# Performance work log

Hardware: AMD Instinct MI355X
Metric: run time of the kernel (lower is better)

The kernel has to match this reference:

```python
import jax, jax.numpy as jnp
import numpy as np
from jax import lax

B, H, W, C, K, R, CB = 2, 128, 128, 256, 64, 8, 256


def _conv(x, w, b=None, pad=1, lhs_dil=None, groups=1):
    out = lax.conv_general_dilated(x, w, (1, 1), [(pad, pad), (pad, pad)],
                                   lhs_dilation=lhs_dil, feature_group_count=groups,
                                   dimension_numbers=('NCHW', 'OIHW', 'NCHW'))
    return out if b is None else out + b[None, :, None, None]


def _silu(x):
    return x * jax.nn.sigmoid(x)


def _fuse(l0, l1, l2, p1w, p1b, p2w, p3w):
    # proj1: Conv(k=3)+SiLU (BN folded); proj2/proj3: grouped ConvTranspose2d as lhs-dilated grouped convs
    a = _silu(_conv(l0, p1w, p1b))
    b2 = _conv(l1, p2w, pad=2, lhs_dil=(2, 2), groups=CB)  # ConvT(2CB->CB, k4, s2, p1, g=CB)
    b3 = _conv(l2, p3w, pad=5, lhs_dil=(4, 4), groups=CB)  # ConvT(4CB->CB, k8, s4, p2, g=CB)
    return a + b2 + b3


def _corr_map(emb, trk):
    # emb: [H,W,C], trk: [K,C]; cosine-similarity correlation with local argmax radius masking
    e = emb / jnp.maximum(jnp.linalg.norm(emb, axis=-1, keepdims=True), 1e-12)
    t = trk / jnp.maximum(jnp.linalg.norm(trk, axis=-1, keepdims=True), 1e-12)
    y = jnp.maximum(jnp.einsum('hwc,kc->khw', e, t), 0.0)  # torch.where(y>0, y, 0)
    idx = jnp.argmax(y.reshape(K, -1), axis=1)             # first max, like torch.nonzero(...)[0]
    ai, aj = idx // W, idx % W
    rows = jnp.arange(H)[None, :, None]
    cols = jnp.arange(W)[None, None, :]
    m = ((rows >= (ai[:, None, None] - R)) & (rows < (ai[:, None, None] + R)) &
         (cols >= (aj[:, None, None] - R)) & (cols < (aj[:, None, None] + R)))
    s = jnp.sum(y * m, axis=0)
    return s / jnp.max(s)


def setup_inputs():
    key = jax.random.key(0)
    ks = jax.random.split(key, 32)
    r = lambda i, shp, s=0.02: jax.random.normal(ks[i], shp, jnp.float32) * s
    z = lambda n: jnp.zeros((n,), jnp.float32)
    return dict(
        id_embeding=jax.random.normal(ks[0], (B, H, W, C), jnp.float32),
        tracklets=jax.random.normal(ks[1], (B, K, C), jnp.float32),
        l0=jax.random.normal(ks[2], (B, CB, H, W), jnp.float32),
        l1=jax.random.normal(ks[3], (B, 2 * CB, H // 2, W // 2), jnp.float32),
        l2=jax.random.normal(ks[4], (B, 4 * CB, H // 4, W // 4), jnp.float32),
        b_p1w=r(5, (CB, CB, 3, 3)), b_p1b=z(CB),
        b_p2w=r(6, (CB, 2, 4, 4)), b_p3w=r(7, (CB, 4, 8, 8)),
        b_c1w=r(8, (CB, CB, 3, 3)), b_c1b=z(CB),
        b_c2w=r(9, (4, CB, 3, 3)), b_c2b=z(4),
        h_p1w=r(10, (CB, CB, 3, 3)), h_p1b=z(CB),
        h_p2w=r(11, (CB, 2, 4, 4)), h_p3w=r(12, (CB, 4, 8, 8)),
        h_c1aw=r(13, (CB, 1, 3, 3), 0.1), h_c1ab=z(CB),
        h_c1bw=r(14, (1, CB, 3, 3)), h_c1bb=z(1),
        h_c2aw=r(15, (CB, CB, 3, 3)), h_c2ab=z(CB),
        h_c2bw=r(16, (CB, CB, 3, 3)), h_c2bb=z(CB),
        h_c2cw=r(17, (1, CB, 3, 3)), h_c2cb=z(1),
    )


def reference(id_embeding, tracklets, l0, l1, l2,
              b_p1w, b_p1b, b_p2w, b_p3w, b_c1w, b_c1b, b_c2w, b_c2b,
              h_p1w, h_p1b, h_p2w, h_p3w,
              h_c1aw, h_c1ab, h_c1bw, h_c1bb,
              h_c2aw, h_c2ab, h_c2bw, h_c2bb, h_c2cw, h_c2cb):
    # correlation map per batch -> x_F [B,1,H,W]
    x_F = jax.vmap(_corr_map)(id_embeding, tracklets)[:, None]
    # recheck_Box head
    xd_box = _fuse(l0, l1, l2, b_p1w, b_p1b, b_p2w, b_p3w)
    xb = _silu(_conv(xd_box, b_c1w, b_c1b))
    siambox = jnp.transpose(_conv(xb, b_c2w, b_c2b), (0, 2, 3, 1))  # [B,H,W,4]
    # recheck_heatmap head
    xd_hm = _fuse(l0, l1, l2, h_p1w, h_p1b, h_p2w, h_p3w)
    xf = _conv(_silu(_conv(x_F, h_c1aw, h_c1ab)), h_c1bw, h_c1bb)   # [B,1,H,W]
    t = xf * xd_hm                                                  # broadcast over CB channels
    t = _silu(_conv(t, h_c2aw, h_c2ab))
    t = _silu(_conv(t, h_c2bw, h_c2bb))
    hmmap = jax.nn.sigmoid(_conv(t, h_c2cw, h_c2cb))                # [B,1,H,W]
    return (hmmap, siambox)
```

## Files before the change

### kernel.cpp

```cpp
#include <hip/hip_runtime.h>
#include <math.h>

#define HH 128
#define WW 128
#define HWSZ 16384
#define CC 256
#define KK 64
#define BB 2

typedef __bf16 bf16x8_t __attribute__((ext_vector_type(8)));
typedef float  f32x4_t  __attribute__((ext_vector_type(4)));

__device__ __forceinline__ float silu_f(float v) { return v / (1.f + expf(-v)); }
__device__ __forceinline__ float sigm_f(float v) { return 1.f / (1.f + expf(-v)); }

__device__ __forceinline__ float b2f(unsigned short u) {
    union { unsigned int i; float f; } x; x.i = ((unsigned int)u) << 16; return x.f;
}
__device__ __forceinline__ unsigned short f2b(float f) {
    union { float f; unsigned int i; } x; x.f = f;
    unsigned int r = x.i + 0x7FFFu + ((x.i >> 16) & 1u);
    return (unsigned short)(r >> 16);
}
__device__ __forceinline__ float u2f(unsigned int u) {
    union { unsigned int i; float f; } x; x.i = u; return x.f;
}

__global__ __launch_bounds__(256) void cvt_nhwc_kernel(const float* __restrict__ in,
                                                       unsigned short* __restrict__ out,
                                                       unsigned long long* __restrict__ ymax,
                                                       unsigned int* __restrict__ umax) {
    __shared__ float T[32][128];
    const int tid = threadIdx.x;
    if (blockIdx.x == 0) {
        if (tid < BB * KK) ymax[tid] = 0ull;
        if (tid >= 128 && tid < 128 + BB) umax[tid - 128] = 0u;
    }
    const int y = blockIdx.x & 127;
    const int b = blockIdx.x >> 7;
    const float* inb = in + (size_t)b * CC * HWSZ + y * 128;
    unsigned short* outb = out + ((size_t)b * HWSZ + (size_t)y * 128) * CC;

    for (int c0 = 0; c0 < CC; c0 += 32) {
        __syncthreads();
        {
            int cl = tid >> 3;
            int xq = tid & 7;
            const float4* src = (const float4*)(inb + (size_t)(c0 + cl) * HWSZ);
            float4* dst = (float4*)&T[cl][0];
            #pragma unroll
            for (int j = 0; j < 4; j++) dst[xq * 4 + j] = src[xq * 4 + j];
        }
        __syncthreads();
        {
            int x = tid & 127, ch = tid >> 7;
            union { unsigned short u[16]; uint4 v[2]; } pk;
            #pragma unroll
            for (int j = 0; j < 16; j++) pk.u[j] = f2b(T[ch * 16 + j][x]);
            uint4* dst = (uint4*)&outb[(size_t)x * CC + c0 + ch * 16];
            dst[0] = pk.v[0];
            dst[1] = pk.v[1];
        }
    }
}

#define WTSZ (9 * 8 * 256 * 32)
__global__ __launch_bounds__(256) void wprep5_kernel(const float* __restrict__ w0,
                                                     const float* __restrict__ w1,
                                                     const float* __restrict__ w2,
                                                     const float* __restrict__ w3,
                                                     const float* __restrict__ w4,
                                                     unsigned short* __restrict__ wtbase) {
    const float* ws[5] = {w0, w1, w2, w3, w4};
    int set = blockIdx.y;
    const float* w = ws[set];
    int idx = blockIdx.x * 256 + threadIdx.x;
    int e   = idx & 7;
    int co  = (idx >> 3) & 255;
    int g   = (idx >> 11) & 3;
    int v   = idx >> 13;
    int cb  = v / 9;
    int t   = v - cb * 9;
    wtbase[(size_t)set * WTSZ + idx] = f2b(w[((size_t)co * 256 + cb * 32 + g * 8 + e) * 9 + t]);
}

#define EPAD 260
__global__ __launch_bounds__(256) void ycorr_kernel(const float* __restrict__ emb,
                                                    const float* __restrict__ trk,
                                                    float* __restrict__ y,
                                                    unsigned long long* __restrict__ ymax) {
    __shared__ __align__(16) float E[64 * EPAD];
    __shared__ __align__(16) float T[64 * EPAD];
    __shared__ float SE[64];
    __shared__ float ST[64];

    const int tid = threadIdx.x;
    const int b   = blockIdx.y;
    const int hw0 = blockIdx.x * 64;

    const float4* esrc = (const float4*)(emb + ((size_t)b * HWSZ + hw0) * CC);
    #pragma unroll
    for (int i = 0; i < 16; i++) {
        int q  = tid + i * 256;
        int px = q >> 6, c4 = q & 63;
        *(float4*)&E[px * EPAD + c4 * 4] = esrc[(size_t)px * 64 + c4];
    }
    const float4* tsrc = (const float4*)(trk + (size_t)b * KK * CC);
    #pragma unroll
    for (int i = 0; i < 16; i++) {
        int q = tid + i * 256;
        int k = q >> 6, c4 = q & 63;
        *(float4*)&T[k * EPAD + c4 * 4] = tsrc[(size_t)k * 64 + c4];
    }
    __syncthreads();

    if (tid < 64) {
        float ss = 0.f;
        const float4* ep = (const float4*)&E[tid * EPAD];
        #pragma unroll 8
        for (int c4 = 0; c4 < 64; c4++) {
            float4 v = ep[c4];
            ss += v.x * v.x + v.y * v.y + v.z * v.z + v.w * v.w;
        }
        SE[tid] = 1.f / fmaxf(sqrtf(ss), 1e-12f);
    } else if (tid < 128) {
        float ss = 0.f;
        const float4* tp = (const float4*)&T[(tid - 64) * EPAD];
        #pragma unroll 8
        for (int c4 = 0; c4 < 64; c4++) {
            float4 v = tp[c4];
            ss += v.x * v.x + v.y * v.y + v.z * v.z + v.w * v.w;
        }
        ST[tid - 64] = 1.f / fmaxf(sqrtf(ss), 1e-12f);
    }
    __syncthreads();

    const int pg = tid & 15;
    const int kg = tid >> 4;

    float acc[4][4];
    #pragma unroll
    for (int jp = 0; jp < 4; jp++)
        #pragma unroll
        for (int jk = 0; jk < 4; jk++) acc[jp][jk] = 0.f;

    const float* Ep[4];
    const float* Tp[4];
    #pragma unroll
    for (int jp = 0; jp < 4; jp++) Ep[jp] = &E[(jp * 16 + pg) * EPAD];
    #pragma unroll
    for (int jk = 0; jk < 4; jk++) Tp[jk] = &T[(jk * 16 + kg) * EPAD];

    #pragma unroll 2
    for (int c4 = 0; c4 < 64; ++c4) {
        float4 e[4], t[4];
        #pragma unroll
        for (int jp = 0; jp < 4; jp++) e[jp] = *(const float4*)(Ep[jp] + c4 * 4);
        #pragma unroll
        for (int jk = 0; jk < 4; jk++) t[jk] = *(const float4*)(Tp[jk] + c4 * 4);
        #define DOT4(a, t) (fmaf(a.w, t.w, fmaf(a.z, t.z, fmaf(a.y, t.y, a.x * t.x))))
        #pragma unroll
        for (int jp = 0; jp < 4; jp++)
            #pragma unroll
            for (int jk = 0; jk < 4; jk++)
                acc[jp][jk] += DOT4(e[jp], t[jk]);
        #undef DOT4
    }

    #pragma unroll
    for (int jk = 0; jk < 4; jk++) {
        int k = jk * 16 + kg;
        float st = ST[k];
        unsigned long long best = 0ull;
        #pragma unroll
        for (int jp = 0; jp < 4; jp++) {
            int px = jp * 16 + pg;
            float val = fmaxf(acc[jp][jk], 0.f) * SE[px] * st;
            y[((size_t)b * KK + k) * HWSZ + hw0 + px] = val;
            union { float f; unsigned int i; } u; u.f = val;
            unsigned long long pk =
                ((unsigned long long)u.i << 32) | (unsigned)(HWSZ - 1 - (hw0 + px));
            best = best > pk ? best : pk;
        }
        #pragma unroll
        for (int m = 1; m < 16; m <<= 1) {
            unsigned long long o = __shfl_xor(best, m);
            best = best > o ? best : o;
        }
        if (pg == 0) atomicMax(&ymax[b * KK + k], best);
    }
}

__global__ __launch_bounds__(256) void smap_kernel(const float* __restrict__ y,
                                                   const unsigned long long* __restrict__ ymax,
                                                   float* __restrict__ s,
                                                   unsigned int* __restrict__ umax) {
    int b  = blockIdx.y;
    int hw = blockIdx.x * 256 + threadIdx.x;
    int h  = hw >> 7, w = hw & 127;
    __shared__ int ai[KK], aj[KK];
    if (threadIdx.x < KK) {
        unsigned long long p = ymax[b * KK + threadIdx.x];
        int v = HWSZ - 1 - (int)(p & 0xFFFFFFFFull);
        ai[threadIdx.x] = v >> 7;
        aj[threadIdx.x] = v & 127;
    }
    __syncthreads();
    const float* yb = y + (size_t)b * KK * HWSZ;
    float acc = 0.f;
    #pragma unroll 8
    for (int k = 0; k < KK; k++) {
        float v = yb[(size_t)k * HWSZ + hw];
        bool in = (h >= ai[k] - 8) && (h < ai[k] + 8) && (w >= aj[k] - 8) && (w < aj[k] + 8);
        acc += in ? v : 0.f;
    }
    s[(size_t)b * HWSZ + hw] = acc;

    __shared__ float sm[256];
    sm[threadIdx.x] = acc;
    __syncthreads();
    for (int st = 128; st > 0; st >>= 1) {
        if (threadIdx.x < st) sm[threadIdx.x] = fmaxf(sm[threadIdx.x], sm[threadIdx.x + st]);
        __syncthreads();
    }
    if (threadIdx.x == 0) {
        union { float f; unsigned int i; } x; x.f = sm[0];
        atomicMax(&umax[b], x.i);
    }
}

template <int HEADS>
__global__ __launch_bounds__(256) void deconv_kernel(const float* __restrict__ l1,
                                                     const float* __restrict__ l2,
                                                     const float* __restrict__ w2a,
                                                     const float* __restrict__ w3a,
                                                     const float* __restrict__ w2b,
                                                     const float* __restrict__ w3b,
                                                     unsigned short* __restrict__ outA,
                                                     unsigned short* __restrict__ outB) {
    __shared__ float L1[2][64][64];
    __shared__ float L2[4][32][32];

    const int tid = threadIdx.x;
    const int g   = blockIdx.x & 255;
    const int b   = blockIdx.x >> 8;

    const float4* l1b = (const float4*)(l1 + ((size_t)b * 2 * CC + 2 * g) * 4096);
    float4* L1p = (float4*)&L1[0][0][0];
    #pragma unroll
    for (int i = 0; i < 8; i++) L1p[tid + i * 256] = l1b[tid + i * 256];
    const float4* l2b = (const float4*)(l2 + ((size_t)b * 4 * CC + 4 * g) * 1024);
    float4* L2p = (float4*)&L2[0][0][0];
    #pragma unroll
    for (int i = 0; i < 4; i++) L2p[tid + i * 256] = l2b[tid + i * 256];

    const int x    = tid & 127;
    const int ytop = tid >> 7;

    const int pxo = x & 1, pyo = ytop & 1;
    const int mx0 = (x + pxo - 2) >> 1;
    const int dy2 = (ytop + pyo - 2) >> 1;
    const bool nok0 = (unsigned)mx0 < 64u;
    const bool nok1 = (unsigned)(mx0 + 1) < 64u;
    const int nc0 = mx0 & 63, nc1 = (mx0 + 1) & 63;

    const int px3 = (5 - (x & 3)) & 3;
    const int n30 = (x + px3 - 5) >> 2;
    const bool n3ok0 = (unsigned)n30 < 32u;
    const bool n3ok1 = (unsigned)(n30 + 1) < 32u;
    const int n3c0 = n30 & 31, n3c1 = (n30 + 1) & 31;
    int dy3[2], py3v[2];
    #pragma unroll
    for (int ph = 0; ph < 2; ph++) {
        int py3 = (5 - ((ytop + 2 * ph) & 3)) & 3;
        py3v[ph] = py3;
        dy3[ph] = (2 * ph + ytop + py3 - 5) >> 2;
    }

    __syncthreads();

    const float* w2s[2] = {w2a, w2b};
    const float* w3s[2] = {w3a, w3b};
    unsigned short* outs[2] = {outA, outB};

    #pragma unroll 1
    for (int hd = 0; hd < HEADS; ++hd) {
        const float* w2g = w2s[hd] + (size_t)g * 32;
        const float* w3g = w3s[hd] + (size_t)g * 256;

        float W2[2][2][2];
        #pragma unroll
        for (int ci = 0; ci < 2; ci++)
            #pragma unroll
            for (int a = 0; a < 2; a++)
                #pragma unroll
                for (int c = 0; c < 2; c++)
                    W2[ci][a][c] = w2g[ci * 16 + (pyo + 2 * a) * 4 + (pxo + 2 * c)];
        float W3[2][4][2][2];
        #pragma unroll
        for (int ph = 0; ph < 2; ph++)
            #pragma unroll
            for (int ci = 0; ci < 4; ci++)
                #pragma unroll
                for (int a = 0; a < 2; a++)
                    #pragma unroll
                    for (int c = 0; c < 2; c++)
                        W3[ph][ci][a][c] = w3g[ci * 64 + (py3v[ph] + 4 * a) * 8 + (px3 + 4 * c)];

        unsigned short* outb = outs[hd] + ((size_t)b * CC + g) * HWSZ;

        #pragma unroll 2
        for (int ii = 0; ii < 32; ++ii) {
            #pragma unroll
            for (int ph = 0; ph < 2; ph++) {
                const int i = 2 * ii + ph;
                float acc = 0.f;
                {
                    const int m0 = i + dy2;
                    #pragma unroll
                    for (int a = 0; a < 2; a++) {
                        int m = m0 + a;
                        bool mok = (unsigned)m < 64u;
                        int mc = m & 63;
                        #pragma unroll
                        for (int ci = 0; ci < 2; ci++) {
                            float v0 = (mok && nok0) ? L1[ci][mc][nc0] : 0.f;
                            float v1 = (mok && nok1) ? L1[ci][mc][nc1] : 0.f;
                            acc = fmaf(W2[ci][a][0], v0, acc);
                            acc = fmaf(W2[ci][a][1], v1, acc);
                        }
                    }
                }
                {
                    const int m0 = ii + dy3[ph];
                    #pragma unroll
                    for (int a = 0; a < 2; a++) {
                        int m = m0 + a;
                        bool mok = (unsigned)m < 32u;
                        int mc = m & 31;
                        #pragma unroll
                        for (int ci = 0; ci < 4; ci++) {
                            float v0 = (mok && n3ok0) ? L2[ci][mc][n3c0] : 0.f;
                            float v1 = (mok && n3ok1) ? L2[ci][mc][n3c1] : 0.f;
                            acc = fmaf(W3[ph][ci][a][0], v0, acc);
                            acc = fmaf(W3[ph][ci][a][1], v1, acc);
                        }
                    }
                }
                outb[(size_t)i * 256 + tid] = f2b(acc);
            }
        }
    }
}

template <int ADDB, int MULF>
__device__ __forceinline__ void conv_mfma_body(
    int y0, int co0, int b,
    const unsigned short* __restrict__ in,
    const unsigned short* __restrict__ wt,
    const float* __restrict__ bias,
    const unsigned short* __restrict__ addb,
    const float* __restrict__ xf,
    unsigned short* __restrict__ out,
    unsigned short (*Alds)[3 * 130 * 32])
{
    const int tid  = threadIdx.x;
    const int lane = tid & 63;
    const int wv   = tid >> 6;
    const int wco  = wv >> 1;
    const int wpx  = wv & 1;
    const int l15  = lane & 15;
    const int kg   = lane >> 4;

    const unsigned short* inb = in + (size_t)b * HWSZ * CC;
    const float* xfb = MULF ? (xf + (size_t)b * HWSZ) : nullptr;
    const unsigned short* wp = wt + (size_t)kg * 2048 + (size_t)(co0 + wco * 64 + l15) * 8;

    int ach[3][4];
    #pragma unroll
    for (int tl = 0; tl < 3; tl++)
        #pragma unroll
        for (int f = 0; f < 4; f++) {
            int px = wpx * 64 + f * 16 + l15 + tl;
            ach[tl][f] = (px * 4 + (kg ^ ((px >> 1) & 3))) * 8;
        }

    f32x4_t acc[4][4];
    #pragma unroll
    for (int i = 0; i < 4; i++)
        #pragma unroll
        for (int j = 0; j < 4; j++)
            acc[i][j] = (f32x4_t){0.f, 0.f, 0.f, 0.f};

    if (tid < 48) {
        int q4 = tid & 3;
        int hp = (tid >> 2) & 1;
        int r  = (tid >> 3) % 3;
        int bi = tid / 24;
        int px = hp ? 129 : 0;
        int chunk = (r * 130 + px) * 4 + (q4 ^ ((px >> 1) & 3));
        *reinterpret_cast<uint4*>(&Alds[bi][chunk * 8]) = make_uint4(0u, 0u, 0u, 0u);
    }

    uint4 streg[6];
    float sxf[6];

    auto load_A = [&](int cb) {
        #pragma unroll
        for (int i = 0; i < 6; i++) {
            int q   = tid + i * 256;
            int q4  = q & 3;
            int pxi = (q >> 2) & 127;
            int r   = q >> 9;
            int gy  = y0 - 1 + r;
            uint4 v = make_uint4(0u, 0u, 0u, 0u);
            float fxv = 0.f;
            if ((unsigned)gy < 128u) {
                v = *reinterpret_cast<const uint4*>(
                        inb + ((size_t)(gy * 128 + pxi)) * CC + cb * 32 + q4 * 8);
                if (MULF) fxv = xfb[gy * 128 + pxi];
            }
            streg[i] = v;
            if (MULF) sxf[i] = fxv;
        }
    };
    auto write_A = [&](int bufi) {
        #pragma unroll
        for (int i = 0; i < 6; i++) {
            int q   = tid + i * 256;
            int q4  = q & 3;
            int pxi = (q >> 2) & 127;
            int r   = q >> 9;
            int px  = pxi + 1;
            int chunk = (r * 130 + px) * 4 + (q4 ^ ((px >> 1) & 3));
            uint4 v = streg[i];
            if (MULF) {
                union { unsigned short u[8]; uint4 w; } pk;
                pk.w = v;
                float fm = sxf[i];
                #pragma unroll
                for (int e = 0; e < 8; e++) pk.u[e] = f2b(b2f(pk.u[e]) * fm);
                v = pk.w;
            }
            *reinterpret_cast<uint4*>(&Alds[bufi][chunk * 8]) = v;
        }
    };

    load_A(0);
    write_A(0);

    bf16x8_t W[3][4], P[2][4];
    #pragma unroll
    for (int f = 0; f < 4; f++) W[0][f] = *reinterpret_cast<const bf16x8_t*>(wp + f * 128);
    #pragma unroll
    for (int f = 0; f < 4; f++) W[1][f] = *reinterpret_cast<const bf16x8_t*>(wp + 8192 + f * 128);

    __syncthreads();
    #pragma unroll
    for (int f = 0; f < 4; f++)
        P[0][f] = *reinterpret_cast<const bf16x8_t*>(&Alds[0][ach[0][f]]);

    for (int cb = 0; cb < 8; ++cb) {
        const int bufi = cb & 1;
        if (cb + 1 < 8) load_A(cb + 1);
        const unsigned short* wcb = wp + (size_t)cb * 73728;
        #pragma unroll
        for (int t = 0; t < 9; ++t) {
            if (cb < 7 || t < 7) {
                #pragma unroll
                for (int f = 0; f < 4; f++)
                    W[(t + 2) % 3][f] = *reinterpret_cast<const bf16x8_t*>(
                        wcb + (t + 2) * 8192 + f * 128);
            }
            if (t < 8) {
                const int aoff = ((t + 1) / 3) * 4160;
                #pragma unroll
                for (int f = 0; f < 4; f++)
                    P[(t + 1) & 1][f] = *reinterpret_cast<const bf16x8_t*>(
                        &Alds[bufi][aoff + ach[(t + 1) % 3][f]]);
            }
            __builtin_amdgcn_sched_barrier(0);
            #pragma unroll
            for (int cf = 0; cf < 4; cf++)
                #pragma unroll
                for (int pf = 0; pf < 4; pf++)
                    acc[cf][pf] = __builtin_amdgcn_mfma_f32_16x16x32_bf16(
                        W[t % 3][cf], P[t & 1][pf], acc[cf][pf], 0, 0, 0);
        }
        if (cb + 1 < 8) write_A(bufi ^ 1);
        __syncthreads();
        if (cb + 1 < 8) {
            #pragma unroll
            for (int f = 0; f < 4; f++)
                P[0][f] = *reinterpret_cast<const bf16x8_t*>(&Alds[(cb + 1) & 1][ach[0][f]]);
        }
    }

    size_t outB = ((size_t)b * HWSZ + (size_t)y0 * 128) * CC;
    #pragma unroll
    for (int cf = 0; cf < 4; cf++) {
        int co = co0 + wco * 64 + cf * 16 + kg * 4;
        float bs0 = bias[co], bs1 = bias[co + 1], bs2 = bias[co + 2], bs3 = bias[co + 3];
        #pragma unroll
        for (int pf = 0; pf < 4; pf++) {
            int x = wpx * 64 + pf * 16 + l15;
            float v0 = silu_f(acc[cf][pf][0] + bs0);
            float v1 = silu_f(acc[cf][pf][1] + bs1);
            float v2 = silu_f(acc[cf][pf][2] + bs2);
            float v3 = silu_f(acc[cf][pf][3] + bs3);
            if (ADDB) {
                size_t ab = ((size_t)b * CC + co) * HWSZ + (size_t)y0 * 128 + x;
                v0 += b2f(addb[ab]);
                v1 += b2f(addb[ab + HWSZ]);
                v2 += b2f(addb[ab + 2 * HWSZ]);
                v3 += b2f(addb[ab + 3 * HWSZ]);
            }
            union { unsigned short u[4]; uint2 v; } pk;
            pk.u[0] = f2b(v0); pk.u[1] = f2b(v1); pk.u[2] = f2b(v2); pk.u[3] = f2b(v3);
            *reinterpret_cast<uint2*>(&out[outB + (size_t)x * CC + co]) = pk.v;
        }
    }
}

template <int ADDB, int MULF>
__global__ __launch_bounds__(256, 2) void conv_mfma_kernel(
    const unsigned short* __restrict__ in,
    const unsigned short* __restrict__ wt,
    const float* __restrict__ bias,
    const unsigned short* __restrict__ addb,
    const float* __restrict__ xf,
    unsigned short* __restrict__ out)
{
    __shared__ __align__(16) unsigned short Alds[2][3 * 130 * 32];
    const int l   = (blockIdx.x & 7) * 64 + (blockIdx.x >> 3);
    const int y0  = l >> 2;
    const int co0 = ((l >> 1) & 1) * 128;
    const int b   = l & 1;
    conv_mfma_body<ADDB, MULF>(y0, co0, b, in, wt, bias, addb, xf, out, Alds);
}

__global__ __launch_bounds__(256, 2) void conv_mfma_dual_kernel(
    const unsigned short* __restrict__ in,
    const unsigned short* __restrict__ wt2set,
    const float* __restrict__ biasB,
    const float* __restrict__ biasH,
    const unsigned short* __restrict__ addbB,
    const unsigned short* __restrict__ addbH,
    unsigned short* __restrict__ outB,
    unsigned short* __restrict__ outH)
{
    __shared__ __align__(16) unsigned short Alds[2][3 * 130 * 32];
    const int l    = (blockIdx.x & 7) * 128 + (blockIdx.x >> 3);
    const int y0   = l >> 3;
    const int c3   = l & 7;
    const int head = c3 >> 2;
    const int co0  = ((c3 >> 1) & 1) * 128;
    const int b    = c3 & 1;
    conv_mfma_body<1, 0>(y0, co0, b,
                         in,
                         wt2set + (size_t)head * WTSZ,
                         head ? biasH : biasB,
                         head ? addbH : addbB,
                         nullptr,
                         head ? outH : outB,
                         Alds);
}

__global__ __launch_bounds__(256, 2) void conv_mfma_dualmix_kernel(
    const unsigned short* __restrict__ in0,
    const unsigned short* __restrict__ in1,
    const unsigned short* __restrict__ wt0,
    const unsigned short* __restrict__ wt1,
    const float* __restrict__ bias0,
    const float* __restrict__ bias1,
    const float* __restrict__ xf,
    unsigned short* __restrict__ out0,
    unsigned short* __restrict__ out1)
{
    __shared__ __align__(16) unsigned short Alds[2][3 * 130 * 32];
    const int l    = (blockIdx.x & 7) * 128 + (blockIdx.x >> 3);
    const int y0   = l >> 3;
    const int c3   = l & 7;
    const int head = c3 >> 2;
    const int co0  = ((c3 >> 1) & 1) * 128;
    const int b    = c3 & 1;
    if (head == 0)
        conv_mfma_body<0, 0>(y0, co0, b, in0, wt0, bias0, nullptr, nullptr, out0, Alds);
    else
        conv_mfma_body<0, 1>(y0, co0, b, in1, wt1, bias1, nullptr, xf, out1, Alds);
}

__global__ __launch_bounds__(256) void conv_c1a_kernel(const float* __restrict__ s,
                                                       const unsigned int* __restrict__ umax,
                                                       const float* __restrict__ w,
                                                       const float* __restrict__ bias,
                                                       unsigned short* __restrict__ out) {
    __shared__ float W[2304];
    __shared__ float S[3][34];

    const int tid = threadIdx.x;
    const int idx = blockIdx.x;
    const int b   = idx >> 9;
    const int seg = idx & 511;
    const int y   = seg >> 2;
    const int x0  = (seg & 3) * 32;

    for (int i = tid; i < 2304; i += 256) W[i] = w[i];
    if (tid < 102) {
        int r = tid / 34, xx = tid - r * 34;
        int gy = y - 1 + r, gx = x0 - 1 + xx;
        S[r][xx] = ((unsigned)gy < 128u && (unsigned)gx < 128u)
                       ? s[(size_t)b * HWSZ + gy * 128 + gx] : 0.f;
    }
    __syncthreads();

    const float im = 1.f / u2f(umax[b]);
    const int cog = tid >> 5;
    const int px  = tid & 31;

    float sv[9];
    #pragma unroll
    for (int r = 0; r < 3; r++)
        #pragma unroll
        for (int d = 0; d < 3; d++)
            sv[r * 3 + d] = S[r][px + d];

    unsigned short* op =
        &out[((size_t)b * HWSZ + (size_t)y * 128 + x0 + px) * CC + cog * 32];
    #pragma unroll
    for (int q = 0; q < 4; q++) {
        union { unsigned short u[8]; uint4 v; } pk;
        #pragma unroll
        for (int j = 0; j < 8; j++) {
            int co = cog * 32 + q * 8 + j;
            float a = 0.f;
            #pragma unroll
            for (int t = 0; t < 9; t++) a = fmaf(W[co * 9 + t], sv[t], a);
            pk.u[j] = f2b(silu_f(a * im + bias[co]));
        }
        *reinterpret_cast<uint4*>(op + q * 8) = pk.v;
    }
}

template <int COUT, int MODE>
__global__ __launch_bounds__(256) void small_conv_kernel(
    const unsigned short* __restrict__ in,
    const float* __restrict__ w,
    const float* __restrict__ bias,
    float* __restrict__ out)
{
    __shared__ float WL[COUT * 9 * 32 * 12];

    const int tid = threadIdx.x;
    for (int i = tid; i < COUT * 2304; i += 256) {
        int e = i & 7;
        int g = (i >> 3) & 31;
        int rest = i >> 8;
        int t = rest % 9;
        int co = rest / 9;
        WL[((co * 9 + t) * 32 + g) * 12 + e] = w[((size_t)co * 256 + g * 8 + e) * 9 + t];
    }
    __syncthreads();

    const int lane = tid & 63;
    const int wv   = tid >> 6;
    const int c32  = lane & 31;
    const int ps   = lane >> 5;
    const int grp  = blockIdx.x * 4 + wv;
    const int base = grp * 4;
    const int b    = base >> 14;
    const int pix  = base & (HWSZ - 1);
    const int y    = pix >> 7;
    const int x0   = pix & 127;
    const int p0x  = x0 + 2 * ps;

    const unsigned short* inb = in + (size_t)b * HWSZ * CC;

    uint4 d[3][4];
    #pragma unroll
    for (int r = 0; r < 3; r++) {
        int gy = y - 1 + r;
        #pragma unroll
        for (int cx = 0; cx < 4; cx++) {
            int gx = p0x - 1 + cx;
            uint4 v = make_uint4(0u, 0u, 0u, 0u);
            if ((unsigned)gy < 128u && (unsigned)gx < 128u)
                v = *reinterpret_cast<const uint4*>(
                        inb + ((size_t)(gy * 128 + gx)) * CC + c32 * 8);
            d[r][cx] = v;
        }
    }

    float acc[2][COUT];
    #pragma unroll
    for (int p = 0; p < 2; p++)
        #pragma unroll
        for (int c = 0; c < COUT; c++) acc[p][c] = 0.f;

    #pragma unroll
    for (int r = 0; r < 3; r++) {
        float f[4][8];
        #pragma unroll
        for (int cx = 0; cx < 4; cx++) {
            union { unsigned short u[8]; uint4 v; } pk;
            pk.v = d[r][cx];
            #pragma unroll
            for (int e = 0; e < 8; e++) f[cx][e] = b2f(pk.u[e]);
        }
        #pragma unroll
        for (int dx = 0; dx < 3; dx++) {
            #pragma unroll
            for (int co = 0; co < COUT; co++) {
                int bse = ((co * 9 + r * 3 + dx) * 32 + c32) * 12;
                float4 wa = *(const float4*)&WL[bse];
                float4 wb = *(const float4*)&WL[bse + 4];
                #pragma unroll
                for (int p = 0; p < 2; p++) {
                    const float* ff = f[dx + p];
                    float a = acc[p][co];
                    a = fmaf(ff[0], wa.x, a); a = fmaf(ff[1], wa.y, a);
                    a = fmaf(ff[2], wa.z, a); a = fmaf(ff[3], wa.w, a);
                    a = fmaf(ff[4], wb.x, a); a = fmaf(ff[5], wb.y, a);
                    a = fmaf(ff[6], wb.z, a); a = fmaf(ff[7], wb.w, a);
                    acc[p][co] = a;
                }
            }
        }
    }

    #pragma unroll
    for (int m = 1; m <= 16; m <<= 1)
        #pragma unroll
        for (int p = 0; p < 2; p++)
            #pragma unroll
            for (int co = 0; co < COUT; co++)
                acc[p][co] += __shfl_xor(acc[p][co], m);

    if (c32 == 0) {
        #pragma unroll
        for (int p = 0; p < 2; p++) {
            size_t pixidx = (size_t)base + 2 * ps + p;
            if (MODE == 0) {
                ((float4*)out)[pixidx] = make_float4(
                    acc[p][0] + bias[0],
                    acc[p][COUT > 1 ? 1 : 0] + bias[COUT > 1 ? 1 : 0],
                    acc[p][COUT > 2 ? 2 : 0] + bias[COUT > 2 ? 2 : 0],
                    acc[p][COUT > 3 ? 3 : 0] + bias[COUT > 3 ? 3 : 0]);
            } else if (MODE == 1) {
                out[pixidx] = acc[p][0] + bias[0];
            } else {
                out[pixidx] = sigm_f(acc[p][0] + bias[0]);
            }
        }
    }
}

extern "C" void kernel_launch(void* const* d_in, const int* in_sizes, int n_in,
                              void* d_out, int out_size, void* d_ws, size_t ws_size,
                              hipStream_t stream) {
    const float* emb    = (const float*)d_in[0];
    const float* trk    = (const float*)d_in[1];
    const float* l0     = (const float*)d_in[2];
    const float* l1     = (const float*)d_in[3];
    const float* l2     = (const float*)d_in[4];
    const float* b_p1w  = (const float*)d_in[5];
    const float* b_p1b  = (const float*)d_in[6];
    const float* b_p2w  = (const float*)d_in[7];
    const float* b_p3w  = (const float*)d_in[8];
    const float* b_c1w  = (const float*)d_in[9];
    const float* b_c1b  = (const float*)d_in[10];
    const float* b_c2w  = (const float*)d_in[11];
    const float* b_c2b  = (const float*)d_in[12];
    const float* h_p1w  = (const float*)d_in[13];
    const float* h_p1b  = (const float*)d_in[14];
    const float* h_p2w  = (const float*)d_in[15];
    const float* h_p3w  = (const float*)d_in[16];
    const float* h_c1aw = (const float*)d_in[17];
    const float* h_c1ab = (const float*)d_in[18];
    const float* h_c1bw = (const float*)d_in[19];
    const float* h_c1bb = (const float*)d_in[20];
    const float* h_c2aw = (const float*)d_in[21];
    const float* h_c2ab = (const float*)d_in[22];
    const float* h_c2bw = (const float*)d_in[23];
    const float* h_c2bb = (const float*)d_in[24];
    const float* h_c2cw = (const float*)d_in[25];
    const float* h_c2cb = (const float*)d_in[26];

    float* outp = (float*)d_out;

    const size_t ACT = (size_t)BB * CC * HWSZ;
    const size_t WT  = (size_t)WTSZ;
    const size_t SMALLS = 132096;

    unsigned short* l0nh = (unsigned short*)d_ws;
    unsigned short* wtP  = l0nh + ACT;
    unsigned short* bufA = wtP + 5 * WT;
    unsigned short* bufB = bufA + ACT;
    unsigned short* bufC = bufB + ACT;
    float* sbuf   = (float*)(bufC + ACT);
    float* xfb    = sbuf + (size_t)BB * HWSZ;
    unsigned long long* ymax = (unsigned long long*)(xfb + (size_t)BB * HWSZ);
    unsigned int* umax = (unsigned int*)(ymax + BB * KK);
    unsigned short* bufD = bufC + ACT + SMALLS;
    float* ybuf   = (float*)bufB;

    const size_t NEED = (size_t)(bufD + ACT - l0nh) * sizeof(unsigned short);
    const bool fast = ws_size >= NEED;

    cvt_nhwc_kernel<<<BB * 128, 256, 0, stream>>>(l0, l0nh, ymax, umax);
    wprep5_kernel<<<dim3((unsigned)(WT / 256), 5), 256, 0, stream>>>(
        b_p1w, h_p1w, b_c1w, h_c2aw, h_c2bw, wtP);

    ycorr_kernel<<<dim3(256, BB), 256, 0, stream>>>(emb, trk, ybuf, ymax);
    smap_kernel<<<dim3(64, BB), 256, 0, stream>>>(ybuf, ymax, sbuf, umax);

    if (fast) {
        deconv_kernel<2><<<BB * CC, 256, 0, stream>>>(l1, l2, b_p2w, b_p3w, h_p2w, h_p3w,
                                                      bufA, bufD);
        conv_mfma_dual_kernel<<<1024, 256, 0, stream>>>(l0nh, wtP, b_p1b, h_p1b,
                                                        bufA, bufD, bufB, bufC);
        conv_c1a_kernel<<<1024, 256, 0, stream>>>(sbuf, umax, h_c1aw, h_c1ab, bufA);
        small_conv_kernel<1, 1><<<2048, 256, 0, stream>>>(bufA, h_c1bw, h_c1bb, xfb);
        conv_mfma_dualmix_kernel<<<1024, 256, 0, stream>>>(bufB, bufC,
                                                           wtP + 2 * WT, wtP + 3 * WT,
                                                           b_c1b, h_c2ab, xfb,
                                                           bufD, bufA);
        small_conv_kernel<4, 0><<<2048, 256, 0, stream>>>(bufD, b_c2w, b_c2b,
                                                          outp + BB * HWSZ);
        conv_mfma_kernel<0, 0><<<512, 256, 0, stream>>>(bufA, wtP + 4 * WT, h_c2bb,
                                                        nullptr, nullptr, bufB);
        small_conv_kernel<1, 2><<<2048, 256, 0, stream>>>(bufB, h_c2cw, h_c2cb, outp);
    } else {
        deconv_kernel<1><<<BB * CC, 256, 0, stream>>>(l1, l2, b_p2w, b_p3w,
                                                      nullptr, nullptr, bufA, nullptr);
        conv_mfma_kernel<1, 0><<<512, 256, 0, stream>>>(l0nh, wtP, b_p1b, bufA,
                                                        nullptr, bufB);
        conv_mfma_kernel<0, 0><<<512, 256, 0, stream>>>(bufB, wtP + 2 * WT, b_c1b,
                                                        nullptr, nullptr, bufC);
        small_conv_kernel<4, 0><<<2048, 256, 0, stream>>>(bufC, b_c2w, b_c2b,
                                                          outp + BB * HWSZ);
        deconv_kernel<1><<<BB * CC, 256, 0, stream>>>(l1, l2, h_p2w, h_p3w,
                                                      nullptr, nullptr, bufA, nullptr);
        conv_mfma_kernel<1, 0><<<512, 256, 0, stream>>>(l0nh, wtP + 1 * WT, h_p1b, bufA,
                                                        nullptr, bufB);
        conv_c1a_kernel<<<1024, 256, 0, stream>>>(sbuf, umax, h_c1aw, h_c1ab, bufC);
        small_conv_kernel<1, 1><<<2048, 256, 0, stream>>>(bufC, h_c1bw, h_c1bb, xfb);
        conv_mfma_kernel<0, 1><<<512, 256, 0, stream>>>(bufB, wtP + 3 * WT, h_c2ab,
                                                        nullptr, xfb, bufA);
        conv_mfma_kernel<0, 0><<<512, 256, 0, stream>>>(bufA, wtP + 4 * WT, h_c2bb,
                                                        nullptr, nullptr, bufC);
        small_conv_kernel<1, 2><<<2048, 256, 0, stream>>>(bufC, h_c2cw, h_c2cb, outp);
    }
}
```

Measured before the change: 395.7 us.

## Merge independent kernels into combined launches via block-index dispatch

Independent stages now share launches. The NHWC conversion and weight prep run in one kernel, smap and deconv run in another, and the third head conv runs alongside the 4-channel box conv, with each block picking its stage from its block index. The goal is fewer kernel launches and less tail idle time, since small or low-occupancy stages can overlap with larger ones. The trade-off is that combined kernels take the largest shared-memory footprint and register budget of their parts, which can lower occupancy for the lighter blocks. Buffer use was also reordered so the xfb computation runs before the dual conv.

```diff
diff --git a/kernel.cpp b/kernel.cpp
--- a/kernel.cpp
+++ b/kernel.cpp
@@ -26,18 +26,18 @@
     union { unsigned int i; float f; } x; x.i = u; return x.f;
 }
 
-__global__ __launch_bounds__(256) void cvt_nhwc_kernel(const float* __restrict__ in,
-                                                       unsigned short* __restrict__ out,
-                                                       unsigned long long* __restrict__ ymax,
-                                                       unsigned int* __restrict__ umax) {
-    __shared__ float T[32][128];
+__device__ __forceinline__ void cvt_nhwc_body(int bid, float (*T)[128],
+                                              const float* __restrict__ in,
+                                              unsigned short* __restrict__ out,
+                                              unsigned long long* __restrict__ ymax,
+                                              unsigned int* __restrict__ umax) {
     const int tid = threadIdx.x;
-    if (blockIdx.x == 0) {
+    if (bid == 0) {
         if (tid < BB * KK) ymax[tid] = 0ull;
         if (tid >= 128 && tid < 128 + BB) umax[tid - 128] = 0u;
     }
-    const int y = blockIdx.x & 127;
-    const int b = blockIdx.x >> 7;
+    const int y = bid & 127;
+    const int b = bid >> 7;
     const float* inb = in + (size_t)b * CC * HWSZ + y * 128;
     unsigned short* outb = out + ((size_t)b * HWSZ + (size_t)y * 128) * CC;
 
@@ -65,16 +65,13 @@
 }
 
 #define WTSZ (9 * 8 * 256 * 32)
-__global__ __launch_bounds__(256) void wprep5_kernel(const float* __restrict__ w0,
-                                                     const float* __restrict__ w1,
-                                                     const float* __restrict__ w2,
-                                                     const float* __restrict__ w3,
-                                                     const float* __restrict__ w4,
-                                                     unsigned short* __restrict__ wtbase) {
-    const float* ws[5] = {w0, w1, w2, w3, w4};
-    int set = blockIdx.y;
+__device__ __forceinline__ void wprep_body(int L,
+                                           const float* const* ws,
+                                           unsigned short* __restrict__ wtbase) {
+    int set = L / 2304;
+    int blk = L - set * 2304;
     const float* w = ws[set];
-    int idx = blockIdx.x * 256 + threadIdx.x;
+    int idx = blk * 256 + threadIdx.x;
     int e   = idx & 7;
     int co  = (idx >> 3) & 255;
     int g   = (idx >> 11) & 3;
@@ -82,6 +79,23 @@
     int cb  = v / 9;
     int t   = v - cb * 9;
     wtbase[(size_t)set * WTSZ + idx] = f2b(w[((size_t)co * 256 + cb * 32 + g * 8 + e) * 9 + t]);
+}
+
+__global__ __launch_bounds__(256) void prep_fused_kernel(
+    const float* __restrict__ l0, unsigned short* __restrict__ l0nh,
+    unsigned long long* __restrict__ ymax, unsigned int* __restrict__ umax,
+    const float* __restrict__ w0, const float* __restrict__ w1,
+    const float* __restrict__ w2, const float* __restrict__ w3,
+    const float* __restrict__ w4, unsigned short* __restrict__ wtbase)
+{
+    __shared__ float T[32][128];
+    const int bid = blockIdx.x;
+    if (bid < 256) {
+        cvt_nhwc_body(bid, T, l0, l0nh, ymax, umax);
+    } else {
+        const float* ws[5] = {w0, w1, w2, w3, w4};
+        wprep_body(bid - 256, ws, wtbase);
+    }
 }
 
 #define EPAD 260
@@ -191,14 +205,18 @@
     }
 }
 
-__global__ __launch_bounds__(256) void smap_kernel(const float* __restrict__ y,
-                                                   const unsigned long long* __restrict__ ymax,
-                                                   float* __restrict__ s,
-                                                   unsigned int* __restrict__ umax) {
-    int b  = blockIdx.y;
-    int hw = blockIdx.x * 256 + threadIdx.x;
+__device__ __forceinline__ void smap_body(int bid, char* smem,
+                                          const float* __restrict__ y,
+                                          const unsigned long long* __restrict__ ymax,
+                                          float* __restrict__ s,
+                                          unsigned int* __restrict__ umax) {
+    int* ai = (int*)smem;
+    int* aj = (int*)(smem + 256);
+    float* sm = (float*)(smem + 512);
+
+    int b  = bid >> 6;
+    int hw = (bid & 63) * 256 + threadIdx.x;
     int h  = hw >> 7, w = hw & 127;
-    __shared__ int ai[KK], aj[KK];
     if (threadIdx.x < KK) {
         unsigned long long p = ymax[b * KK + threadIdx.x];
         int v = HWSZ - 1 - (int)(p & 0xFFFFFFFFull);
@@ -216,7 +234,6 @@
     }
     s[(size_t)b * HWSZ + hw] = acc;
 
-    __shared__ float sm[256];
     sm[threadIdx.x] = acc;
     __syncthreads();
     for (int st = 128; st > 0; st >>= 1) {
@@ -230,20 +247,21 @@
 }
 
 template <int HEADS>
-__global__ __launch_bounds__(256) void deconv_kernel(const float* __restrict__ l1,
-                                                     const float* __restrict__ l2,
-                                                     const float* __restrict__ w2a,
-                                                     const float* __restrict__ w3a,
-                                                     const float* __restrict__ w2b,
-                                                     const float* __restrict__ w3b,
-                                                     unsigned short* __restrict__ outA,
-                                                     unsigned short* __restrict__ outB) {
-    __shared__ float L1[2][64][64];
-    __shared__ float L2[4][32][32];
+__device__ __forceinline__ void deconv_body(int bid, char* smem,
+                                            const float* __restrict__ l1,
+                                            const float* __restrict__ l2,
+                                            const float* __restrict__ w2a,
+                                            const float* __restrict__ w3a,
+                                            const float* __restrict__ w2b,
+                                            const float* __restrict__ w3b,
+                                            unsigned short* __restrict__ outA,
+                                            unsigned short* __restrict__ outB) {
+    float (*L1)[64][64] = (float (*)[64][64])smem;
+    float (*L2)[32][32] = (float (*)[32][32])(smem + 32768);
 
     const int tid = threadIdx.x;
-    const int g   = blockIdx.x & 255;
-    const int b   = blockIdx.x >> 8;
+    const int g   = bid & 255;
+    const int b   = bid >> 8;
 
     const float4* l1b = (const float4*)(l1 + ((size_t)b * 2 * CC + 2 * g) * 4096);
     float4* L1p = (float4*)&L1[0][0][0];
@@ -353,6 +371,40 @@
     }
 }
 
+__global__ __launch_bounds__(256) void smap_kernel(const float* __restrict__ y,
+                                                   const unsigned long long* __restrict__ ymax,
+                                                   float* __restrict__ s,
+                                                   unsigned int* __restrict__ umax) {
+    __shared__ __align__(16) char smem[1536];
+    smap_body(blockIdx.x, smem, y, ymax, s, umax);
+}
+template <int HEADS>
+__global__ __launch_bounds__(256) void deconv_kernel(const float* __restrict__ l1,
+                                                     const float* __restrict__ l2,
+                                                     const float* __restrict__ w2a,
+                                                     const float* __restrict__ w3a,
+                                                     const float* __restrict__ w2b,
+                                                     const float* __restrict__ w3b,
+                                                     unsigned short* __restrict__ outA,
+                                                     unsigned short* __restrict__ outB) {
+    __shared__ __align__(16) char smem[49152];
+    deconv_body<HEADS>(blockIdx.x, smem, l1, l2, w2a, w3a, w2b, w3b, outA, outB);
+}
+
+__global__ __launch_bounds__(256) void smapdeconv_kernel(
+    const float* __restrict__ y, const unsigned long long* __restrict__ ymax,
+    float* __restrict__ s, unsigned int* __restrict__ umax,
+    const float* __restrict__ l1, const float* __restrict__ l2,
+    const float* __restrict__ w2a, const float* __restrict__ w3a,
+    const float* __restrict__ w2b, const float* __restrict__ w3b,
+    unsigned short* __restrict__ outA, unsigned short* __restrict__ outB)
+{
+    __shared__ __align__(16) char smem[49152];
+    const int bid = blockIdx.x;
+    if (bid < 128) smap_body(bid, smem, y, ymax, s, umax);
+    else           deconv_body<2>(bid - 128, smem, l1, l2, w2a, w3a, w2b, w3b, outA, outB);
+}
+
 template <int ADDB, int MULF>
 __device__ __forceinline__ void conv_mfma_body(
     int y0, int co0, int b,
@@ -556,14 +608,9 @@
     const int head = c3 >> 2;
     const int co0  = ((c3 >> 1) & 1) * 128;
     const int b    = c3 & 1;
-    conv_mfma_body<1, 0>(y0, co0, b,
-                         in,
-                         wt2set + (size_t)head * WTSZ,
-                         head ? biasH : biasB,
-                         head ? addbH : addbB,
-                         nullptr,
-                         head ? outH : outB,
-                         Alds);
+    conv_mfma_body<1, 0>(y0, co0, b, in, wt2set + (size_t)head * WTSZ,
+                         head ? biasH : biasB, head ? addbH : addbB,
+                         nullptr, head ? outH : outB, Alds);
 }
 
 __global__ __launch_bounds__(256, 2) void conv_mfma_dualmix_kernel(
@@ -643,14 +690,12 @@
 }
 
 template <int COUT, int MODE>
-__global__ __launch_bounds__(256) void small_conv_kernel(
-    const unsigned short* __restrict__ in,
-    const float* __restrict__ w,
-    const float* __restrict__ bias,
-    float* __restrict__ out)
+__device__ __forceinline__ void small_conv_body(int bid, float* WL,
+                                                const unsigned short* __restrict__ in,
+                                                const float* __restrict__ w,
+                                                const float* __restrict__ bias,
+                                                float* __restrict__ out)
 {
-    __shared__ float WL[COUT * 9 * 32 * 12];
-
     const int tid = threadIdx.x;
     for (int i = tid; i < COUT * 2304; i += 256) {
         int e = i & 7;
@@ -666,7 +711,7 @@
     const int wv   = tid >> 6;
     const int c32  = lane & 31;
     const int ps   = lane >> 5;
-    const int grp  = blockIdx.x * 4 + wv;
+    const int grp  = bid * 4 + wv;
     const int base = grp * 4;
     const int b    = base >> 14;
     const int pix  = base & (HWSZ - 1);
@@ -752,6 +797,41 @@
                 out[pixidx] = sigm_f(acc[p][0] + bias[0]);
             }
         }
+    }
+}
+
+template <int COUT, int MODE>
+__global__ __launch_bounds__(256) void small_conv_kernel(
+    const unsigned short* __restrict__ in,
+    const float* __restrict__ w,
+    const float* __restrict__ bias,
+    float* __restrict__ out)
+{
+    __shared__ float WL[COUT * 9 * 32 * 12];
+    small_conv_body<COUT, MODE>(blockIdx.x, WL, in, w, bias, out);
+}
+
+__global__ __launch_bounds__(256, 2) void t3c2_kernel(
+    const unsigned short* __restrict__ t2in,
+    const unsigned short* __restrict__ wt4,
+    const float* __restrict__ biasT3,
+    unsigned short* __restrict__ t3out,
+    const unsigned short* __restrict__ xbin,
+    const float* __restrict__ c2w,
+    const float* __restrict__ c2b,
+    float* __restrict__ boxout)
+{
+    __shared__ __align__(16) char smem[55296];
+    const int bid = blockIdx.x;
+    if (bid < 512) {
+        const int l   = (bid & 7) * 64 + (bid >> 3);
+        const int y0  = l >> 2;
+        const int co0 = ((l >> 1) & 1) * 128;
+        const int b   = l & 1;
+        conv_mfma_body<0, 0>(y0, co0, b, t2in, wt4, biasT3, nullptr, nullptr, t3out,
+                             (unsigned short (*)[3 * 130 * 32])smem);
+    } else {
+        small_conv_body<4, 0>(bid - 512, (float*)smem, xbin, c2w, c2b, boxout);
     }
 }
 
@@ -807,30 +887,29 @@
     const size_t NEED = (size_t)(bufD + ACT - l0nh) * sizeof(unsigned short);
     const bool fast = ws_size >= NEED;
 
-    cvt_nhwc_kernel<<<BB * 128, 256, 0, stream>>>(l0, l0nh, ymax, umax);
-    wprep5_kernel<<<dim3((unsigned)(WT / 256), 5), 256, 0, stream>>>(
-        b_p1w, h_p1w, b_c1w, h_c2aw, h_c2bw, wtP);
+    prep_fused_kernel<<<256 + 11520, 256, 0, stream>>>(
+        l0, l0nh, ymax, umax, b_p1w, h_p1w, b_c1w, h_c2aw, h_c2bw, wtP);
 
     ycorr_kernel<<<dim3(256, BB), 256, 0, stream>>>(emb, trk, ybuf, ymax);
-    smap_kernel<<<dim3(64, BB), 256, 0, stream>>>(ybuf, ymax, sbuf, umax);
 
     if (fast) {
-        deconv_kernel<2><<<BB * CC, 256, 0, stream>>>(l1, l2, b_p2w, b_p3w, h_p2w, h_p3w,
-                                                      bufA, bufD);
+        smapdeconv_kernel<<<128 + 512, 256, 0, stream>>>(
+            ybuf, ymax, sbuf, umax,
+            l1, l2, b_p2w, b_p3w, h_p2w, h_p3w, bufA, bufD);
+        conv_c1a_kernel<<<1024, 256, 0, stream>>>(sbuf, umax, h_c1aw, h_c1ab, bufB);
+        small_conv_kernel<1, 1><<<2048, 256, 0, stream>>>(bufB, h_c1bw, h_c1bb, xfb);
         conv_mfma_dual_kernel<<<1024, 256, 0, stream>>>(l0nh, wtP, b_p1b, h_p1b,
                                                         bufA, bufD, bufB, bufC);
-        conv_c1a_kernel<<<1024, 256, 0, stream>>>(sbuf, umax, h_c1aw, h_c1ab, bufA);
-        small_conv_kernel<1, 1><<<2048, 256, 0, stream>>>(bufA, h_c1bw, h_c1bb, xfb);
         conv_mfma_dualmix_kernel<<<1024, 256, 0, stream>>>(bufB, bufC,
                                                            wtP + 2 * WT, wtP + 3 * WT,
                                                            b_c1b, h_c2ab, xfb,
                                                            bufD, bufA);
-        small_conv_kernel<4, 0><<<2048, 256, 0, stream>>>(bufD, b_c2w, b_c2b,
-                                                          outp + BB * HWSZ);
-        conv_mfma_kernel<0, 0><<<512, 256, 0, stream>>>(bufA, wtP + 4 * WT, h_c2bb,
-                                                        nullptr, nullptr, bufB);
+        t3c2_kernel<<<512 + 2048, 256, 0, stream>>>(bufA, wtP + 4 * WT, h_c2bb, bufB,
+                                                    bufD, b_c2w, b_c2b,
+                                                    outp + BB * HWSZ);
         small_conv_kernel<1, 2><<<2048, 256, 0, stream>>>(bufB, h_c2cw, h_c2cb, outp);
     } else {
+        smap_kernel<<<64 * BB, 256, 0, stream>>>(ybuf, ymax, sbuf, umax);
         deconv_kernel<1><<<BB * CC, 256, 0, stream>>>(l1, l2, b_p2w, b_p3w,
                                                       nullptr, nullptr, bufA, nullptr);
         conv_mfma_kernel<1, 0><<<512, 256, 0, stream>>>(l0nh, wtP, b_p1b, bufA,
```

Result: faster. 376.0 us, median of 5 (-5.0%).
